# Kernel tuning notes

Measured on AMD Instinct MI355X. Metric: run time of the kernel, lower is better.

Reference implementation:

```python
import jax, jax.numpy as jnp
import numpy as np

DIM = 4096
DIM_OUTS = (4096, 4096, 4096)
R = 8
SCALE = 1.0  # alpha defaults to r -> alpha/r = 1


def setup_inputs() -> dict:
    key = jax.random.key(0)
    ks = jax.random.split(key, 1 + len(DIM_OUTS))
    x = jax.random.normal(ks[0], (4, 4096, DIM), dtype=jnp.float32)
    # A ~ randn, B ~ zeros per torch init; use small randn for B so grads/outputs are nontrivial? 
    # Faithful to module init: B = zeros. Keep zeros.
    As = [jax.random.normal(ks[1 + i], (DIM, R), dtype=jnp.float32) for i in range(len(DIM_OUTS))]
    Bs = [jnp.zeros((R, d), dtype=jnp.float32) for d in DIM_OUTS]
    return {
        "x": x,
        "A0": As[0], "B0": Bs[0],
        "A1": As[1], "B1": Bs[1],
        "A2": As[2], "B2": Bs[2],
    }


def reference(x, A0, B0, A1, B1, A2, B2):
    # Faithful math: x @ concat([A_i @ B_i * scale], axis=-1)
    # Efficient form: compute (x @ A_i) @ B_i * scale per LoRA, then concat.
    # Same Rs allow stacking into one batched low-rank chain.
    A = jnp.stack([A0, A1, A2])          # [L, dim, r]
    B = jnp.stack([B0, B1, B2])          # [L, r, dim_out]
    xa = jnp.einsum('bsd,ldr->lbsr', x, A)   # [L, B, S, r]
    out = jnp.einsum('lbsr,lro->lbso', xa, B) * SCALE  # [L, B, S, dim_out]
    # concat along last dim in lora order
    L, Bb, S, O = out.shape
    return jnp.moveaxis(out, 0, 2).reshape(Bb, S, L * O)
```

## Files before the change

kernel.cpp:

```cpp
#include <hip/hip_runtime.h>


#define DIM       4096
#define M_ROWS    16384
#define RANK      8
#define NC        24
#define OUT_COLS  12288

typedef float floatx4 __attribute__((ext_vector_type(4)));

#define KC             512
#define ROWS_PER_WAVE  2
#define ROWS_PER_BLOCK 8

__launch_bounds__(256, 3)
__global__ void lora_xa_kernel(const float* __restrict__ x,
                               const float* __restrict__ A0,
                               const float* __restrict__ A1,
                               const float* __restrict__ A2,
                               float* __restrict__ xa) {
  __shared__ float At[NC][KC];

  const int tid  = threadIdx.x;
  const int lane = tid & 63;
  const int wave = tid >> 6;
  const int row0 = blockIdx.x * ROWS_PER_BLOCK + wave * ROWS_PER_WAVE;

  float acc[ROWS_PER_WAVE][NC];
#pragma unroll
  for (int r = 0; r < ROWS_PER_WAVE; ++r)
#pragma unroll
    for (int c = 0; c < NC; ++c) acc[r][c] = 0.f;

  for (int kb = 0; kb < DIM; kb += KC) {
    float4 xv[2][ROWS_PER_WAVE];
#pragma unroll
    for (int step = 0; step < 2; ++step)
#pragma unroll
      for (int r = 0; r < ROWS_PER_WAVE; ++r)
        xv[step][r] = *(const float4*)(x + (size_t)(row0 + r) * DIM + kb +
                                       step * 256 + 4 * lane);

#pragma unroll
    for (int j = 0; j < 12; ++j) {
      const int l   = j >> 2;
      const int idx = tid + (j & 3) * 256;
      const int dof = idx >> 1;
      const int rq  = (idx & 1) * 4;
      const float* Ap = (l == 0) ? A0 : (l == 1) ? A1 : A2;
      const float4 v = *(const float4*)(Ap + (size_t)(kb + dof) * RANK + rq);
      At[l * RANK + rq + 0][dof] = v.x;
      At[l * RANK + rq + 1][dof] = v.y;
      At[l * RANK + rq + 2][dof] = v.z;
      At[l * RANK + rq + 3][dof] = v.w;
    }
    __syncthreads();

#pragma unroll
    for (int step = 0; step < 2; ++step) {
      const int kl = step * 256 + 4 * lane;
#pragma unroll
      for (int c = 0; c < NC; ++c) {
        const float4 av = *(const float4*)(&At[c][kl]);
#pragma unroll
        for (int r = 0; r < ROWS_PER_WAVE; ++r) {
          acc[r][c] = fmaf(xv[step][r].x, av.x, acc[r][c]);
          acc[r][c] = fmaf(xv[step][r].y, av.y, acc[r][c]);
          acc[r][c] = fmaf(xv[step][r].z, av.z, acc[r][c]);
          acc[r][c] = fmaf(xv[step][r].w, av.w, acc[r][c]);
        }
      }
    }
    __syncthreads();
  }

#pragma unroll
  for (int r = 0; r < ROWS_PER_WAVE; ++r)
#pragma unroll
    for (int c = 0; c < NC; ++c) {
      float v = acc[r][c];
#pragma unroll
      for (int off = 32; off > 0; off >>= 1) v += __shfl_xor(v, off, 64);
      acc[r][c] = v;
    }

  float outv[ROWS_PER_WAVE];
#pragma unroll
  for (int c = 0; c < NC; ++c)
#pragma unroll
    for (int r = 0; r < ROWS_PER_WAVE; ++r)
      if (lane == c) outv[r] = acc[r][c];

  if (lane < NC) {
#pragma unroll
    for (int r = 0; r < ROWS_PER_WAVE; ++r)
      xa[(size_t)(row0 + r) * NC + lane] = outv[r];
  }
}

#define ROW_TILE        128
#define COLS_PER_BLOCK  1024

__launch_bounds__(256, 4)
__global__ void lora_expand_kernel(const float* __restrict__ xa,
                                   const float* __restrict__ B0,
                                   const float* __restrict__ B1,
                                   const float* __restrict__ B2,
                                   float* __restrict__ out) {
  const int ctile = blockIdx.x;
  const int rtile = blockIdx.y;
  const int l     = ctile >> 2;
  const int o     = (ctile & 3) * COLS_PER_BLOCK + threadIdx.x * 4;
  const float* B  = (l == 0) ? B0 : (l == 1) ? B1 : B2;

  float4 b[RANK];
#pragma unroll
  for (int r = 0; r < RANK; ++r)
    b[r] = *(const float4*)(B + (size_t)r * DIM + o);

  const int row0    = rtile * ROW_TILE;
  const size_t ocol = (size_t)l * DIM + o;

#pragma unroll 8
  for (int i = 0; i < ROW_TILE; ++i) {
    const int row = row0 + i;
    const float* xr = xa + (size_t)row * NC + l * RANK;
    const float4 s0 = *(const float4*)(xr);
    const float4 s1 = *(const float4*)(xr + 4);
    const float s[8] = {s0.x, s0.y, s0.z, s0.w, s1.x, s1.y, s1.z, s1.w};

    floatx4 acc = {0.f, 0.f, 0.f, 0.f};
#pragma unroll
    for (int r = 0; r < RANK; ++r) {
      acc.x = fmaf(s[r], b[r].x, acc.x);
      acc.y = fmaf(s[r], b[r].y, acc.y);
      acc.z = fmaf(s[r], b[r].z, acc.z);
      acc.w = fmaf(s[r], b[r].w, acc.w);
    }
    __builtin_nontemporal_store(acc, (floatx4*)(out + (size_t)row * OUT_COLS + ocol));
  }
}

extern "C" void kernel_launch(void* const* d_in, const int* in_sizes, int n_in,
                              void* d_out, int out_size, void* d_ws, size_t ws_size,
                              hipStream_t stream) {
  const float* x  = (const float*)d_in[0];
  const float* A0 = (const float*)d_in[1];
  const float* B0 = (const float*)d_in[2];
  const float* A1 = (const float*)d_in[3];
  const float* B1 = (const float*)d_in[4];
  const float* A2 = (const float*)d_in[5];
  const float* B2 = (const float*)d_in[6];
  float* out = (float*)d_out;
  float* xa  = (float*)d_ws;

  if (ws_size < (size_t)M_ROWS * NC * sizeof(float)) return;

  lora_xa_kernel<<<dim3(M_ROWS / ROWS_PER_BLOCK), dim3(256), 0, stream>>>(
      x, A0, A1, A2, xa);
  lora_expand_kernel<<<dim3(12, M_ROWS / ROW_TILE), dim3(256), 0, stream>>>(
      xa, B0, B1, B2, out);
}
```

Measured before the change: 1.090 ms.

## Fuse down-projection and up-projection into one kernel via shared-memory xa

Merges the x@A reduction kernel and the xa@B expansion kernel into a single kernel. Each block keeps its 8 rows of xa in shared memory and then writes the full 12288-column output for those rows, which removes the xa workspace round-trip and one launch. It also switches the output stores from nontemporal to regular stores. In exchange, each block now has a long serial write phase after the reduction, and B must be reloaded by every block (2048 blocks) instead of once per column tile.

```diff
diff --git a/kernel.cpp b/kernel.cpp
--- a/kernel.cpp
+++ b/kernel.cpp
@@ -14,17 +14,22 @@
 #define ROWS_PER_BLOCK 8
 
 __launch_bounds__(256, 3)
-__global__ void lora_xa_kernel(const float* __restrict__ x,
-                               const float* __restrict__ A0,
-                               const float* __restrict__ A1,
-                               const float* __restrict__ A2,
-                               float* __restrict__ xa) {
+__global__ void lora_fused_kernel(const float* __restrict__ x,
+                                  const float* __restrict__ A0,
+                                  const float* __restrict__ A1,
+                                  const float* __restrict__ A2,
+                                  const float* __restrict__ B0,
+                                  const float* __restrict__ B1,
+                                  const float* __restrict__ B2,
+                                  float* __restrict__ out) {
   __shared__ float At[NC][KC];
+  __shared__ float sxa[ROWS_PER_BLOCK][NC];
 
   const int tid  = threadIdx.x;
   const int lane = tid & 63;
   const int wave = tid >> 6;
-  const int row0 = blockIdx.x * ROWS_PER_BLOCK + wave * ROWS_PER_WAVE;
+  const int brow = blockIdx.x * ROWS_PER_BLOCK;
+  const int row0 = brow + wave * ROWS_PER_WAVE;
 
   float acc[ROWS_PER_WAVE][NC];
 #pragma unroll
@@ -94,50 +99,39 @@
   if (lane < NC) {
 #pragma unroll
     for (int r = 0; r < ROWS_PER_WAVE; ++r)
-      xa[(size_t)(row0 + r) * NC + lane] = outv[r];
+      sxa[wave * ROWS_PER_WAVE + r][lane] = outv[r];
   }
-}
+  __syncthreads();
 
-#define ROW_TILE        128
-#define COLS_PER_BLOCK  1024
+  const int tid4 = tid * 4;
+#pragma unroll 1
+  for (int g = 0; g < 12; ++g) {
+    const int l = g >> 2;
+    const int o = (g & 3) * 1024 + tid4;
+    const float* B = (l == 0) ? B0 : (l == 1) ? B1 : B2;
 
-__launch_bounds__(256, 4)
-__global__ void lora_expand_kernel(const float* __restrict__ xa,
-                                   const float* __restrict__ B0,
-                                   const float* __restrict__ B1,
-                                   const float* __restrict__ B2,
-                                   float* __restrict__ out) {
-  const int ctile = blockIdx.x;
-  const int rtile = blockIdx.y;
-  const int l     = ctile >> 2;
-  const int o     = (ctile & 3) * COLS_PER_BLOCK + threadIdx.x * 4;
-  const float* B  = (l == 0) ? B0 : (l == 1) ? B1 : B2;
+    float4 b[RANK];
+#pragma unroll
+    for (int r = 0; r < RANK; ++r)
+      b[r] = *(const float4*)(B + (size_t)r * DIM + o);
 
-  float4 b[RANK];
+    const size_t ocol = (size_t)l * DIM + o;
 #pragma unroll
-  for (int r = 0; r < RANK; ++r)
-    b[r] = *(const float4*)(B + (size_t)r * DIM + o);
+    for (int i = 0; i < ROWS_PER_BLOCK; ++i) {
+      const float4 s0 = *(const float4*)(&sxa[i][l * RANK]);
+      const float4 s1 = *(const float4*)(&sxa[i][l * RANK + 4]);
+      const float s[8] = {s0.x, s0.y, s0.z, s0.w, s1.x, s1.y, s1.z, s1.w};
 
-  const int row0    = rtile * ROW_TILE;
-  const size_t ocol = (size_t)l * DIM + o;
-
-#pragma unroll 8
-  for (int i = 0; i < ROW_TILE; ++i) {
-    const int row = row0 + i;
-    const float* xr = xa + (size_t)row * NC + l * RANK;
-    const float4 s0 = *(const float4*)(xr);
-    const float4 s1 = *(const float4*)(xr + 4);
-    const float s[8] = {s0.x, s0.y, s0.z, s0.w, s1.x, s1.y, s1.z, s1.w};
-
-    floatx4 acc = {0.f, 0.f, 0.f, 0.f};
+      floatx4 a4 = {0.f, 0.f, 0.f, 0.f};
 #pragma unroll
-    for (int r = 0; r < RANK; ++r) {
-      acc.x = fmaf(s[r], b[r].x, acc.x);
-      acc.y = fmaf(s[r], b[r].y, acc.y);
-      acc.z = fmaf(s[r], b[r].z, acc.z);
-      acc.w = fmaf(s[r], b[r].w, acc.w);
+      for (int r = 0; r < RANK; ++r) {
+        a4.x = fmaf(s[r], b[r].x, a4.x);
+        a4.y = fmaf(s[r], b[r].y, a4.y);
+        a4.z = fmaf(s[r], b[r].z, a4.z);
+        a4.w = fmaf(s[r], b[r].w, a4.w);
+      }
+      *(floatx4*)(out + (size_t)(brow + i) * OUT_COLS + ocol) = a4;
     }
-    __builtin_nontemporal_store(acc, (floatx4*)(out + (size_t)row * OUT_COLS + ocol));
   }
 }
 
@@ -152,12 +146,7 @@
   const float* A2 = (const float*)d_in[5];
   const float* B2 = (const float*)d_in[6];
   float* out = (float*)d_out;
-  float* xa  = (float*)d_ws;
 
-  if (ws_size < (size_t)M_ROWS * NC * sizeof(float)) return;
-
-  lora_xa_kernel<<<dim3(M_ROWS / ROWS_PER_BLOCK), dim3(256), 0, stream>>>(
-      x, A0, A1, A2, xa);
-  lora_expand_kernel<<<dim3(12, M_ROWS / ROW_TILE), dim3(256), 0, stream>>>(
-      xa, B0, B1, B2, out);
+  lora_fused_kernel<<<dim3(M_ROWS / ROWS_PER_BLOCK), dim3(256), 0, stream>>>(
+      x, A0, A1, A2, B0, B1, B2, out);
 }
```

After: 1.099 ms. About the same (+0.8%).
